# Kernel tuning notes

Hardware: AMD Instinct MI355X
Metric: run time of the kernel (lower is better)

The kernel has to match this reference:

```python
import jax, jax.numpy as jnp
import numpy as np

N = 100000   # nodes
E = 800000   # directed edges (symmetrized to 2E in forward)
D0 = 128     # input feature dim (dim0)
H = 128      # hidden = h_dim * args.d = 64 * 2
L = 4        # num_layers
G = 64       # num graphs for global_mean_pool
BN_EPS = 1e-5
LN_EPS = 1e-5


def setup_inputs() -> dict:
    key = jax.random.key(0)
    ks = jax.random.split(key, 12)
    s = 1.0 / np.sqrt(H)
    x = jax.random.normal(ks[0], (N, D0), dtype=jnp.float32)
    row = jax.random.randint(ks[1], (E,), 0, N, dtype=jnp.int32)
    off = jax.random.randint(ks[2], (E,), 1, N, dtype=jnp.int32)
    col = (row + off) % N  # guarantees row != col (no self loops)
    edge_index = jnp.stack([row, col])
    batch = jnp.sort(jax.random.randint(ks[3], (N,), 0, G, dtype=jnp.int32))
    return {
        "x": x,
        "W0": jax.random.normal(ks[4], (D0, H), dtype=jnp.float32) * s,
        "b0": jnp.zeros((H,), jnp.float32),
        "eps_l": jnp.zeros((L,), jnp.float32),        # GIN eps per layer
        "W1": jax.random.normal(ks[5], (L, H, H), dtype=jnp.float32) * s,
        "b1": jnp.zeros((L, H), jnp.float32),
        "bn_g": jnp.ones((L, H), jnp.float32),
        "bn_b": jnp.zeros((L, H), jnp.float32),
        "W2": jax.random.normal(ks[6], (L, H, H), dtype=jnp.float32) * s,
        "b2": jnp.zeros((L, H), jnp.float32),
        "ln_g": jnp.ones((L, H), jnp.float32),
        "ln_b": jnp.zeros((L, H), jnp.float32),
        "edge_index": edge_index,
        "batch": batch,
    }


def reference(x, W0, b0, eps_l, W1, b1, bn_g, bn_b, W2, b2, ln_g, ln_b, edge_index, batch):
    n = x.shape[0]
    h = x @ W0 + b0  # layer0 encode -> [N, H]
    # FNSD: symmetrize edges (cat with flip) and drop self loops
    ei = jnp.concatenate([edge_index, edge_index[::-1]], axis=1)
    row, col = ei[0], ei[1]
    w = (row != col).astype(h.dtype)  # self-loop removal as zero edge weight
    for i in range(L):
        # GINConv: scatter-add of neighbor features
        agg = jax.ops.segment_sum(w[:, None] * h[col], row, num_segments=n)
        u = (1.0 + eps_l[i]) * h + agg
        # mlp: Linear -> BatchNorm1d (training-mode batch stats) -> ReLU -> Linear
        z = u @ W1[i] + b1[i]
        m = jnp.mean(z, axis=0)
        v = jnp.var(z, axis=0)
        z = (z - m) * jax.lax.rsqrt(v + BN_EPS) * bn_g[i] + bn_b[i]
        z = jax.nn.relu(z)
        z = z @ W2[i] + b2[i]
        z = jax.nn.relu(z)          # use_activation
        h = h + z                    # use_residual
        mu = jnp.mean(h, axis=-1, keepdims=True)   # LayerNorm
        var = jnp.var(h, axis=-1, keepdims=True)
        h = (h - mu) * jax.lax.rsqrt(var + LN_EPS) * ln_g[i] + ln_b[i]
    # global_mean_pool over graph ids
    cnt = jax.ops.segment_sum(jnp.ones((n,), h.dtype), batch, num_segments=G)
    sums = jax.ops.segment_sum(h, batch, num_segments=G)
    return sums / jnp.maximum(cnt, 1.0)[:, None]
```

## Files before the change

### kernel.cpp

```cpp
#include <hip/hip_runtime.h>

#define NN 100000
#define EE 800000
#define HH 128
#define LL 4
#define GG 64
#define BN_EPS 1e-5f
#define LN_EPS 1e-5f
#define POOL_CHUNK 64
#define NBUK ((NN + 255) >> 8)
#define CAP 8192
#define BCHUNK 8192
#define UPITCH 136
#define Q8SCALE 16.0f
#define Q8INV   0.0625f

typedef __attribute__((ext_vector_type(8))) short short8;
typedef __attribute__((ext_vector_type(4))) float f32x4;

__device__ inline unsigned short bf16_rne(float f) {
    unsigned u = __float_as_uint(f);
    return (unsigned short)((u + 0x7FFF + ((u >> 16) & 1)) >> 16);
}
__device__ inline float bf16_to_f32(unsigned short h) {
    return __uint_as_float((unsigned)h << 16);
}


__global__ void setup_kernel(const float* __restrict__ W0, const float* __restrict__ W1,
                             const float* __restrict__ W2, short* __restrict__ wt_hi,
                             int* __restrict__ bcur, float* __restrict__ colsum,
                             float* __restrict__ psum, float* __restrict__ pcnt) {
    int i = blockIdx.x * 256 + threadIdx.x;
    if (i < NBUK) bcur[i] = i * CAP;
    if (i < LL * HH * 2) colsum[i] = 0.f;
    if (i < GG * HH) psum[i] = 0.f;
    if (i < GG) pcnt[i] = 0.f;
    if (i < 9 * HH * HH) {
        int mat = i >> 14, rem = i & 16383;
        int n = rem >> 7, k = rem & 127;
        const float* src = (mat == 0) ? W0 : ((mat <= 4) ? W1 + (size_t)(mat - 1) * HH * HH
                                                         : W2 + (size_t)(mat - 5) * HH * HH);
        float v = src[(size_t)k * HH + n];
        int off = (mat << 14) + (((k >> 3) * 8 + (n >> 4)) << 7) + ((n & 15) << 3) + (k & 7);
        wt_hi[off] = (short)bf16_rne(v);
    }
}


__global__ __launch_bounds__(256) void bucket_scatter(const int* __restrict__ ei, int* __restrict__ bcur,
                                                      int* __restrict__ pairs) {
    __shared__ int h[NBUK];
    __shared__ int curb[NBUK];
    int tid = threadIdx.x;
    for (int i = tid; i < NBUK; i += 256) h[i] = 0;
    __syncthreads();
    int base = blockIdx.x * BCHUNK;
#pragma unroll 4
    for (int k = 0; k < BCHUNK / 256; k++) {
        int e = base + k * 256 + tid;
        if (e < 2 * EE) {
            int r = ei[e];
            int c = (e < EE) ? ei[e + EE] : ei[e - EE];
            if (r != c) atomicAdd(&h[r >> 8], 1);
        }
    }
    __syncthreads();
    for (int i = tid; i < NBUK; i += 256) {
        int n = h[i];
        curb[i] = n ? atomicAdd(&bcur[i], n) : 0;
    }
    __syncthreads();
#pragma unroll 4
    for (int k = 0; k < BCHUNK / 256; k++) {
        int e = base + k * 256 + tid;
        if (e < 2 * EE) {
            int r = ei[e];
            int c = (e < EE) ? ei[e + EE] : ei[e - EE];
            if (r != c) {
                int p = atomicAdd(&curb[r >> 8], 1);
                pairs[p] = ((r & 255) << 17) | c;
            }
        }
    }
}

__global__ __launch_bounds__(256) void bucket_build(const int* __restrict__ pairs, const int* __restrict__ bcur,
                                                    int* __restrict__ rp, int* __restrict__ re,
                                                    int* __restrict__ colidx) {
    __shared__ int hist[256], off[256], lcol[CAP];
    int b = blockIdx.x, tid = threadIdx.x;
    int s = b * CAP;
    int size = bcur[b] - s;
    hist[tid] = 0;
    __syncthreads();
    for (int i = tid; i < size; i += 256) atomicAdd(&hist[pairs[s + i] >> 17], 1);
    __syncthreads();
    off[tid] = hist[tid];
    __syncthreads();
    for (int o = 1; o < 256; o <<= 1) {
        int x = (tid >= o) ? off[tid - o] : 0;
        __syncthreads();
        off[tid] += x;
        __syncthreads();
    }
    int excl = (tid > 0) ? off[tid - 1] : 0;
    int r = (b << 8) + tid;
    if (r < NN) { rp[r] = s + excl; re[r] = s + off[tid]; }
    hist[tid] = excl;
    __syncthreads();
    for (int i = tid; i < size; i += 256) {
        int u = pairs[s + i];
        int p = atomicAdd(&hist[u >> 17], 1);
        lcol[p] = u & 0x1FFFF;
    }
    __syncthreads();
    for (int i = tid; i < size; i += 256) colidx[s + i] = lcol[i];
}


__global__ __launch_bounds__(256, 6) void fused_g1(
    const uint2* __restrict__ hbf2,
    const unsigned int* __restrict__ h8,
    const int* __restrict__ rp, const int* __restrict__ re,
    const int* __restrict__ colidx,
    const float* __restrict__ eps_l, int layer,
    const short* __restrict__ wt,
    const float* __restrict__ bias,
    unsigned short* __restrict__ z1_out,
    float* __restrict__ colsum, float* __restrict__ colsq)
{
    __shared__ __align__(16) unsigned short uls[64 * UPITCH];
    __shared__ float stats[2 * HH];
    int tid = threadIdx.x;
    int wave = tid >> 6, lane = tid & 63;
    int half = lane >> 5, sub = lane & 31;
    int lrow = lane & 15, kgrp = lane >> 4;
    int r0 = blockIdx.x * 64;
    stats[tid] = 0.f;
    float eps1 = 1.0f + eps_l[layer];

    int hw = wave * 2 + half;
    for (int rl = 0; rl < 8; rl++) {
        int row = hw * 8 + rl;
        int r = r0 + row;
        float a0 = 0.f, a1 = 0.f, a2 = 0.f, a3 = 0.f;
        uint2 sv = make_uint2(0u, 0u);
        if (r < NN) {
            sv = hbf2[(size_t)r * 32 + sub];
            int base = rp[r];
            int n = re[r] - base;
            for (int i = 0; i < n; i += 8) {
                unsigned v[8];
                int c[8];
#pragma unroll
                for (int j = 0; j < 8; j++) c[j] = (i + j < n) ? colidx[base + i + j] : -1;
#pragma unroll
                for (int j = 0; j < 8; j++)
                    v[j] = (c[j] >= 0) ? h8[(size_t)c[j] * 32 + sub] : 0u;
#pragma unroll
                for (int j = 0; j < 8; j++) {
                    a0 += (float)((int)(v[j] << 24) >> 24);
                    a1 += (float)((int)(v[j] << 16) >> 24);
                    a2 += (float)((int)(v[j] <<  8) >> 24);
                    a3 += (float)((int)v[j] >> 24);
                }
            }
        }
        a0 = fmaf(bf16_to_f32((unsigned short)(sv.x & 0xFFFF)), eps1, a0 * Q8INV);
        a1 = fmaf(bf16_to_f32((unsigned short)(sv.x >> 16)),    eps1, a1 * Q8INV);
        a2 = fmaf(bf16_to_f32((unsigned short)(sv.y & 0xFFFF)), eps1, a2 * Q8INV);
        a3 = fmaf(bf16_to_f32((unsigned short)(sv.y >> 16)),    eps1, a3 * Q8INV);
        uint2 o;
        o.x = (unsigned)bf16_rne(a0) | ((unsigned)bf16_rne(a1) << 16);
        o.y = (unsigned)bf16_rne(a2) | ((unsigned)bf16_rne(a3) << 16);
        *(uint2*)&uls[row * UPITCH + sub * 4] = o;
    }
    __syncthreads();

    short8 az[4];
#pragma unroll
    for (int ks = 0; ks < 4; ks++)
        az[ks] = *(const short8*)&uls[(wave * 16 + lrow) * UPITCH + ks * 32 + kgrp * 8];
    __syncthreads();

    f32x4 acc[8];
#pragma unroll
    for (int c = 0; c < 8; c++) acc[c] = (f32x4){0.f, 0.f, 0.f, 0.f};
#pragma unroll
    for (int ks = 0; ks < 4; ks++) {
        int fb = (ks * 4 + kgrp) * 8;
#pragma unroll
        for (int c = 0; c < 8; c++) {
            short8 whi = *(const short8*)(wt + (size_t)((fb + c) << 7) + (lrow << 3));
            acc[c] = __builtin_amdgcn_mfma_f32_16x16x32_bf16(az[ks], whi, acc[c], 0, 0, 0);
        }
    }

    float bv[8];
#pragma unroll
    for (int c = 0; c < 8; c++) bv[c] = bias[c * 16 + lrow];
    int lrb = wave * 16 + kgrp * 4;
    float ps[8], pq[8];
#pragma unroll
    for (int c = 0; c < 8; c++) { ps[c] = 0.f; pq[c] = 0.f; }
#pragma unroll
    for (int c = 0; c < 8; c++)
#pragma unroll
        for (int reg = 0; reg < 4; reg++) {
            float z = acc[c][reg] + bv[c];
            uls[(lrb + reg) * UPITCH + c * 16 + lrow] = bf16_rne(z);
            if (r0 + lrb + reg < NN) { ps[c] += z; pq[c] += z * z; }
        }
#pragma unroll
    for (int c = 0; c < 8; c++) {
        ps[c] += __shfl_xor(ps[c], 16); pq[c] += __shfl_xor(pq[c], 16);
        ps[c] += __shfl_xor(ps[c], 32); pq[c] += __shfl_xor(pq[c], 32);
    }
    if (kgrp == 0) {
#pragma unroll
        for (int c = 0; c < 8; c++) {
            atomicAdd(&stats[c * 16 + lrow], ps[c]);
            atomicAdd(&stats[HH + c * 16 + lrow], pq[c]);
        }
    }
    __syncthreads();
#pragma unroll
    for (int i = 0; i < 4; i++) {
        int idx = tid + i * 256;
        int row = idx >> 4;
        int r = r0 + row;
        if (r < NN)
            *(uint4*)(z1_out + (size_t)r * HH + (idx & 15) * 8) =
                *(const uint4*)&uls[row * UPITCH + (idx & 15) * 8];
    }
    if (tid < HH) {
        atomicAdd(&colsum[tid], stats[tid]);
        atomicAdd(&colsq[tid], stats[HH + tid]);
    }
}


template<int MODE>
__global__ __launch_bounds__(256, 4) void gemm_v9(
    const void* __restrict__ Ain,
    const short* __restrict__ wt_hi,
    const float* __restrict__ bias,
    float* __restrict__ colsum, float* __restrict__ colsq,
    const float* __restrict__ bng, const float* __restrict__ bnb,
    const float* __restrict__ lng, const float* __restrict__ lnb,
    unsigned short* __restrict__ hbf,
    unsigned int* __restrict__ h8out)
{
    __shared__ short wh[HH * HH];
    __shared__ float stats[2 * HH];
    int tid = threadIdx.x;
    int wave = tid >> 6, lane = tid & 63;
    int lrow = lane & 15, kgrp = lane >> 4;
    int r0 = blockIdx.x * 64;
    int arow = r0 + wave * 16 + lrow;

    {
        const short8* src = (const short8*)wt_hi;
        short8* dst = (short8*)wh;
#pragma unroll
        for (int i = 0; i < 8; i++) dst[tid + i * 256] = src[tid + i * 256];
    }
    if (MODE == 2 && tid < HH) {
        float m = colsum[tid] * (1.f / NN);
        float v = colsq[tid] * (1.f / NN) - m * m;
        float a = bng[tid] * rsqrtf(v + BN_EPS);
        stats[tid] = a;
        stats[HH + tid] = bnb[tid] - m * a;
    }

    float4 a0[4], a1[4];
    short8 az[4];
    if (MODE == 2) {
        const unsigned short* Az = (const unsigned short*)Ain;
        if (arow < NN) {
#pragma unroll
            for (int ks = 0; ks < 4; ks++)
                az[ks] = *(const short8*)(Az + (size_t)arow * HH + ks * 32 + kgrp * 8);
        } else {
#pragma unroll
            for (int ks = 0; ks < 4; ks++) az[ks] = (short8){0,0,0,0,0,0,0,0};
        }
    } else {
        const float* Af = (const float*)Ain;
        if (arow < NN) {
#pragma unroll
            for (int ks = 0; ks < 4; ks++) {
                int kb = ks * 32 + kgrp * 8;
                a0[ks] = *(const float4*)(Af + (size_t)arow * HH + kb);
                a1[ks] = *(const float4*)(Af + (size_t)arow * HH + kb + 4);
            }
        } else {
#pragma unroll
            for (int ks = 0; ks < 4; ks++) {
                a0[ks] = make_float4(0.f, 0.f, 0.f, 0.f);
                a1[ks] = a0[ks];
            }
        }
    }
    __syncthreads();

    f32x4 acc[8];
#pragma unroll
    for (int c = 0; c < 8; c++) acc[c] = (f32x4){0.f, 0.f, 0.f, 0.f};

#pragma unroll
    for (int ks = 0; ks < 4; ks++) {
        int fb = (ks * 4 + kgrp) * 8;
        int kb = ks * 32 + kgrp * 8;
        float av[8];
        if (MODE == 2) {
#pragma unroll
            for (int j = 0; j < 8; j++) {
                float zb = bf16_to_f32((unsigned short)az[ks][j]);
                av[j] = fmaxf(fmaf(zb, stats[kb + j], stats[HH + kb + j]), 0.f);
            }
        } else {
            av[0] = a0[ks].x; av[1] = a0[ks].y; av[2] = a0[ks].z; av[3] = a0[ks].w;
            av[4] = a1[ks].x; av[5] = a1[ks].y; av[6] = a1[ks].z; av[7] = a1[ks].w;
        }
        short8 ahi, alo;
#pragma unroll
        for (int j = 0; j < 8; j++) {
            unsigned short hb = bf16_rne(av[j]);
            ahi[j] = (short)hb;
            alo[j] = (short)bf16_rne(av[j] - bf16_to_f32(hb));
        }
#pragma unroll
        for (int c = 0; c < 8; c++) {
            short8 whi = *(const short8*)(wh + ((fb + c) << 7) + (lrow << 3));
            acc[c] = __builtin_amdgcn_mfma_f32_16x16x32_bf16(ahi, whi, acc[c], 0, 0, 0);
            acc[c] = __builtin_amdgcn_mfma_f32_16x16x32_bf16(alo, whi, acc[c], 0, 0, 0);
        }
    }

    float bv[8];
#pragma unroll
    for (int c = 0; c < 8; c++) bv[c] = bias[c * 16 + lrow];
    int lrb = wave * 16 + kgrp * 4;
    unsigned short* hst = (unsigned short*)wh;

    if (MODE == 0) {
        __syncthreads();
#pragma unroll
        for (int c = 0; c < 8; c++)
#pragma unroll
            for (int reg = 0; reg < 4; reg++)
                hst[(lrb + reg) * HH + c * 16 + lrow] = bf16_rne(acc[c][reg] + bv[c]);
        __syncthreads();
#pragma unroll
        for (int i = 0; i < 4; i++) {
            int idx = tid + i * 256;
            int r = r0 + (idx >> 4);
            if (r < NN)
                *(uint4*)(hbf + (size_t)r * HH + (idx & 15) * 8) = ((const uint4*)wh)[idx];
        }
    } else {
        float lg[8], lb[8];
#pragma unroll
        for (int c = 0; c < 8; c++) {
            lg[c] = lng[c * 16 + lrow];
            lb[c] = lnb[c * 16 + lrow];
        }
        __syncthreads();
#pragma unroll
        for (int i = 0; i < 4; i++) {
            int idx = tid + i * 256;
            int r = r0 + (idx >> 4);
            uint4 v = make_uint4(0, 0, 0, 0);
            if (r < NN) v = *(const uint4*)(hbf + (size_t)r * HH + (idx & 15) * 8);
            ((uint4*)wh)[idx] = v;
        }
        __syncthreads();
#pragma unroll
        for (int reg = 0; reg < 4; reg++) {
            int r = r0 + lrb + reg;
            if (r < NN) {
                float tv[8];
                float s = 0.f, q = 0.f;
#pragma unroll
                for (int c = 0; c < 8; c++) {
                    float hold = bf16_to_f32(hst[(lrb + reg) * HH + c * 16 + lrow]);
                    tv[c] = hold + fmaxf(acc[c][reg] + bv[c], 0.f);
                    s += tv[c]; q += tv[c] * tv[c];
                }
#pragma unroll
                for (int m = 1; m < 16; m <<= 1) {
                    s += __shfl_xor(s, m);
                    q += __shfl_xor(q, m);
                }
                float mu = s * (1.f / 128.f);
                float var = q * (1.f / 128.f) - mu * mu;
                float rs = rsqrtf(var + LN_EPS);
#pragma unroll
                for (int c = 0; c < 8; c++)
                    hst[(lrb + reg) * HH + c * 16 + lrow] =
                        bf16_rne((tv[c] - mu) * rs * lg[c] + lb[c]);
            }
        }
        __syncthreads();
#pragma unroll
        for (int i = 0; i < 4; i++) {
            int idx = tid + i * 256;
            int r = r0 + (idx >> 4);
            if (r < NN)
                *(uint4*)(hbf + (size_t)r * HH + (idx & 15) * 8) = ((const uint4*)wh)[idx];
        }
    }

    if (h8out) {
#pragma unroll
        for (int i = 0; i < 2; i++) {
            int idx = tid + i * 256;
            int row = idx >> 3, q = idx & 7;
            int r = r0 + row;
            if (r < NN) {
                unsigned w[4];
#pragma unroll
                for (int k = 0; k < 4; k++) {
                    uint2 d = *(const uint2*)&hst[row * HH + q * 16 + k * 4];
                    float f0 = bf16_to_f32((unsigned short)(d.x & 0xFFFF));
                    float f1 = bf16_to_f32((unsigned short)(d.x >> 16));
                    float f2 = bf16_to_f32((unsigned short)(d.y & 0xFFFF));
                    float f3 = bf16_to_f32((unsigned short)(d.y >> 16));
                    int q0 = (int)rintf(fminf(fmaxf(f0 * Q8SCALE, -127.f), 127.f));
                    int q1 = (int)rintf(fminf(fmaxf(f1 * Q8SCALE, -127.f), 127.f));
                    int q2 = (int)rintf(fminf(fmaxf(f2 * Q8SCALE, -127.f), 127.f));
                    int q3 = (int)rintf(fminf(fmaxf(f3 * Q8SCALE, -127.f), 127.f));
                    w[k] = (unsigned)(q0 & 255) | ((unsigned)(q1 & 255) << 8) |
                           ((unsigned)(q2 & 255) << 16) | ((unsigned)(q3 & 255) << 24);
                }
                *(uint4*)(h8out + (size_t)r * 32 + q * 4) = make_uint4(w[0], w[1], w[2], w[3]);
            }
        }
    }
}


__global__ void pool_kernel(const unsigned short* __restrict__ h, const int* __restrict__ batch,
                            float* __restrict__ psum, float* __restrict__ pcnt)
{
    int t = threadIdx.x;
    int n0 = blockIdx.x * POOL_CHUNK;
    int n1 = n0 + POOL_CHUNK; if (n1 > NN) n1 = NN;
    if (n0 >= NN) return;
    float acc = 0.f;
    int cur = batch[n0];
    int cnt = 0;
    for (int n = n0; n < n1; n++) {
        int g = batch[n];
        if (g != cur) {
            atomicAdd(&psum[cur * HH + t], acc);
            if (t == 0) atomicAdd(&pcnt[cur], (float)cnt);
            acc = 0.f; cnt = 0; cur = g;
        }
        acc += bf16_to_f32(h[(size_t)n * HH + t]);
        cnt++;
    }
    atomicAdd(&psum[cur * HH + t], acc);
    if (t == 0) atomicAdd(&pcnt[cur], (float)cnt);
}

__global__ void pool_final(const float* __restrict__ psum, const float* __restrict__ pcnt,
                           float* __restrict__ out)
{
    int i = blockIdx.x * blockDim.x + threadIdx.x;
    if (i < GG * HH) {
        float c = pcnt[i >> 7];
        out[i] = psum[i] / fmaxf(c, 1.f);
    }
}


extern "C" void kernel_launch(void* const* d_in, const int* in_sizes, int n_in,
                              void* d_out, int out_size, void* d_ws, size_t ws_size,
                              hipStream_t stream)
{
    const float* x     = (const float*)d_in[0];
    const float* W0    = (const float*)d_in[1];
    const float* b0    = (const float*)d_in[2];
    const float* eps_l = (const float*)d_in[3];
    const float* W1    = (const float*)d_in[4];
    const float* b1    = (const float*)d_in[5];
    const float* bng   = (const float*)d_in[6];
    const float* bnb   = (const float*)d_in[7];
    const float* W2    = (const float*)d_in[8];
    const float* b2    = (const float*)d_in[9];
    const float* lng   = (const float*)d_in[10];
    const float* lnb   = (const float*)d_in[11];
    const int*   ei    = (const int*)d_in[12];
    const int*   batch = (const int*)d_in[13];
    float* out = (float*)d_out;

    char* ws = (char*)d_ws;
    size_t off = 0;
    auto alloc = [&](size_t bytes) -> void* {
        void* p = ws + off;
        off += (bytes + 255) & ~(size_t)255;
        return p;
    };
    unsigned short* hbf = (unsigned short*)alloc((size_t)NN * HH * 2);
    unsigned short* z1  = (unsigned short*)alloc((size_t)NN * HH * 2);
    unsigned int*   h8  = (unsigned int*)alloc((size_t)NN * HH);
    int*   colidx = (int*)alloc((size_t)NBUK * CAP * 4 + 1024);
    int*   pairs  = (int*)alloc((size_t)NBUK * CAP * 4);
    int*   rp     = (int*)alloc((size_t)NN * 4);
    int*   re     = (int*)alloc((size_t)NN * 4);
    int*   bcur   = (int*)alloc((NBUK + 1) * 4);
    float* colsum = (float*)alloc((size_t)LL * HH * 2 * 4);
    float* psum   = (float*)alloc((size_t)GG * HH * 4);
    float* pcnt   = (float*)alloc(GG * 4);
    short* wt_hi  = (short*)alloc((size_t)9 * HH * HH * 2);

    setup_kernel<<<(9 * HH * HH + 255) / 256, 256, 0, stream>>>(W0, W1, W2, wt_hi, bcur,
                                                                colsum, psum, pcnt);

    bucket_scatter<<<(2 * EE + BCHUNK - 1) / BCHUNK, 256, 0, stream>>>(ei, bcur, pairs);
    bucket_build<<<NBUK, 256, 0, stream>>>(pairs, bcur, rp, re, colidx);

    int gb = (NN + 63) / 64;
    gemm_v9<0><<<gb, 256, 0, stream>>>(x, wt_hi, b0,
                                       nullptr, nullptr, nullptr, nullptr, nullptr, nullptr,
                                       hbf, h8);

    for (int l = 0; l < LL; l++) {
        float* cs = colsum + (size_t)l * HH * 2;
        float* cq = cs + HH;
        fused_g1<<<gb, 256, 0, stream>>>((const uint2*)hbf, h8, rp, re, colidx, eps_l, l,
                                         wt_hi + (size_t)(1 + l) * HH * HH, b1 + l * HH, z1,
                                         cs, cq);
        gemm_v9<2><<<gb, 256, 0, stream>>>(z1, wt_hi + (size_t)(5 + l) * HH * HH,
                                           b2 + l * HH,
                                           cs, cq, bng + l * HH, bnb + l * HH,
                                           lng + l * HH, lnb + l * HH, hbf,
                                           (l < LL - 1) ? h8 : nullptr);
    }

    pool_kernel<<<(NN + POOL_CHUNK - 1) / POOL_CHUNK, 128, 0, stream>>>(hbf, batch, psum, pcnt);
    pool_final<<<(GG * HH + 255) / 256, 256, 0, stream>>>(psum, pcnt, out);
}
```

Baseline: 606.9 us.

## Pad CSR rows to multiples of eight, stage indices in LDS, use packed integer accumulation

Pads each node's neighbor list to a multiple of eight, filling the padding with a dummy node whose int8 features are zero, so the gather loop drops its per-element bounds checks and loads indices as int4 vectors. Each block first copies its contiguous slice of column indices into LDS when the slice fits, and falls back to global memory otherwise. Int8 feature sums use SWAR: a bias XOR plus two 16-bit lanes in a 32-bit add, with the bias subtracted at the end, replacing per-byte float converts. The padding adds extra gather traffic against the dummy row, and the 16-bit lane sums could overflow on very high-degree nodes.

```diff
diff --git a/kernel.cpp b/kernel.cpp
--- a/kernel.cpp
+++ b/kernel.cpp
@@ -14,6 +14,7 @@
 #define UPITCH 136
 #define Q8SCALE 16.0f
 #define Q8INV   0.0625f
+#define CIDX_CAP 2048
 
 typedef __attribute__((ext_vector_type(8))) short short8;
 typedef __attribute__((ext_vector_type(4))) float f32x4;
@@ -30,12 +31,14 @@
 __global__ void setup_kernel(const float* __restrict__ W0, const float* __restrict__ W1,
                              const float* __restrict__ W2, short* __restrict__ wt_hi,
                              int* __restrict__ bcur, float* __restrict__ colsum,
-                             float* __restrict__ psum, float* __restrict__ pcnt) {
+                             float* __restrict__ psum, float* __restrict__ pcnt,
+                             unsigned int* __restrict__ h8) {
     int i = blockIdx.x * 256 + threadIdx.x;
     if (i < NBUK) bcur[i] = i * CAP;
     if (i < LL * HH * 2) colsum[i] = 0.f;
     if (i < GG * HH) psum[i] = 0.f;
     if (i < GG) pcnt[i] = 0.f;
+    if (i < 32) h8[(size_t)NN * 32 + i] = 0u;
     if (i < 9 * HH * HH) {
         int mat = i >> 14, rem = i & 16383;
         int n = rem >> 7, k = rem & 127;
@@ -85,6 +88,7 @@
     }
 }
 
+
 __global__ __launch_bounds__(256) void bucket_build(const int* __restrict__ pairs, const int* __restrict__ bcur,
                                                     int* __restrict__ rp, int* __restrict__ re,
                                                     int* __restrict__ colidx) {
@@ -93,10 +97,12 @@
     int s = b * CAP;
     int size = bcur[b] - s;
     hist[tid] = 0;
+    for (int i = tid; i < CAP; i += 256) lcol[i] = NN;
     __syncthreads();
     for (int i = tid; i < size; i += 256) atomicAdd(&hist[pairs[s + i] >> 17], 1);
     __syncthreads();
-    off[tid] = hist[tid];
+    int p = (hist[tid] + 7) & ~7;
+    off[tid] = p;
     __syncthreads();
     for (int o = 1; o < 256; o <<= 1) {
         int x = (tid >= o) ? off[tid - o] : 0;
@@ -104,18 +110,19 @@
         off[tid] += x;
         __syncthreads();
     }
-    int excl = (tid > 0) ? off[tid - 1] : 0;
+    int pexcl = off[tid] - p;
     int r = (b << 8) + tid;
-    if (r < NN) { rp[r] = s + excl; re[r] = s + off[tid]; }
-    hist[tid] = excl;
+    if (r < NN) { rp[r] = s + pexcl; re[r] = s + pexcl + p; }
+    hist[tid] = pexcl;
     __syncthreads();
     for (int i = tid; i < size; i += 256) {
         int u = pairs[s + i];
-        int p = atomicAdd(&hist[u >> 17], 1);
-        lcol[p] = u & 0x1FFFF;
-    }
-    __syncthreads();
-    for (int i = tid; i < size; i += 256) colidx[s + i] = lcol[i];
+        int pos = atomicAdd(&hist[u >> 17], 1);
+        lcol[pos] = u & 0x1FFFF;
+    }
+    __syncthreads();
+    int ptot = off[255];
+    for (int i = tid; i < ptot; i += 256) colidx[s + i] = lcol[i];
 }
 
 
@@ -131,6 +138,7 @@
     float* __restrict__ colsum, float* __restrict__ colsq)
 {
     __shared__ __align__(16) unsigned short uls[64 * UPITCH];
+    __shared__ __align__(16) int cidx[CIDX_CAP];
     __shared__ float stats[2 * HH];
     int tid = threadIdx.x;
     int wave = tid >> 6, lane = tid & 63;
@@ -140,37 +148,79 @@
     stats[tid] = 0.f;
     float eps1 = 1.0f + eps_l[layer];
 
+    int lastr = r0 + 63; if (lastr >= NN) lastr = NN - 1;
+    int blkBase = rp[r0];
+    int blkSize = re[lastr] - blkBase;
+    bool ldsOk = (blkSize <= CIDX_CAP);
+    if (ldsOk) {
+        const int4* src = (const int4*)(colidx + blkBase);
+        for (int i = tid; i * 4 < blkSize; i += 256) ((int4*)cidx)[i] = src[i];
+    }
+    __syncthreads();
+
     int hw = wave * 2 + half;
     for (int rl = 0; rl < 8; rl++) {
         int row = hw * 8 + rl;
         int r = r0 + row;
-        float a0 = 0.f, a1 = 0.f, a2 = 0.f, a3 = 0.f;
         uint2 sv = make_uint2(0u, 0u);
+        unsigned accLo = 0u, accHi = 0u;
+        int npad = 0;
         if (r < NN) {
             sv = hbf2[(size_t)r * 32 + sub];
             int base = rp[r];
-            int n = re[r] - base;
-            for (int i = 0; i < n; i += 8) {
-                unsigned v[8];
-                int c[8];
-#pragma unroll
-                for (int j = 0; j < 8; j++) c[j] = (i + j < n) ? colidx[base + i + j] : -1;
-#pragma unroll
-                for (int j = 0; j < 8; j++)
-                    v[j] = (c[j] >= 0) ? h8[(size_t)c[j] * 32 + sub] : 0u;
-#pragma unroll
-                for (int j = 0; j < 8; j++) {
-                    a0 += (float)((int)(v[j] << 24) >> 24);
-                    a1 += (float)((int)(v[j] << 16) >> 24);
-                    a2 += (float)((int)(v[j] <<  8) >> 24);
-                    a3 += (float)((int)v[j] >> 24);
+            npad = re[r] - base;
+            if (ldsOk) {
+                int lo = base - blkBase;
+                for (int i = 0; i < npad; i += 8) {
+                    int4 i0 = *(const int4*)&cidx[lo + i];
+                    int4 i1 = *(const int4*)&cidx[lo + i + 4];
+                    unsigned v[8];
+                    v[0] = h8[(size_t)i0.x * 32 + sub];
+                    v[1] = h8[(size_t)i0.y * 32 + sub];
+                    v[2] = h8[(size_t)i0.z * 32 + sub];
+                    v[3] = h8[(size_t)i0.w * 32 + sub];
+                    v[4] = h8[(size_t)i1.x * 32 + sub];
+                    v[5] = h8[(size_t)i1.y * 32 + sub];
+                    v[6] = h8[(size_t)i1.z * 32 + sub];
+                    v[7] = h8[(size_t)i1.w * 32 + sub];
+#pragma unroll
+                    for (int j = 0; j < 8; j++) {
+                        unsigned b = v[j] ^ 0x80808080u;
+                        accLo += b & 0x00FF00FFu;
+                        accHi += (b >> 8) & 0x00FF00FFu;
+                    }
                 }
-            }
-        }
-        a0 = fmaf(bf16_to_f32((unsigned short)(sv.x & 0xFFFF)), eps1, a0 * Q8INV);
-        a1 = fmaf(bf16_to_f32((unsigned short)(sv.x >> 16)),    eps1, a1 * Q8INV);
-        a2 = fmaf(bf16_to_f32((unsigned short)(sv.y & 0xFFFF)), eps1, a2 * Q8INV);
-        a3 = fmaf(bf16_to_f32((unsigned short)(sv.y >> 16)),    eps1, a3 * Q8INV);
+            } else {
+                for (int i = 0; i < npad; i += 8) {
+                    int4 i0 = *(const int4*)&colidx[base + i];
+                    int4 i1 = *(const int4*)&colidx[base + i + 4];
+                    unsigned v[8];
+                    v[0] = h8[(size_t)i0.x * 32 + sub];
+                    v[1] = h8[(size_t)i0.y * 32 + sub];
+                    v[2] = h8[(size_t)i0.z * 32 + sub];
+                    v[3] = h8[(size_t)i0.w * 32 + sub];
+                    v[4] = h8[(size_t)i1.x * 32 + sub];
+                    v[5] = h8[(size_t)i1.y * 32 + sub];
+                    v[6] = h8[(size_t)i1.z * 32 + sub];
+                    v[7] = h8[(size_t)i1.w * 32 + sub];
+#pragma unroll
+                    for (int j = 0; j < 8; j++) {
+                        unsigned b = v[j] ^ 0x80808080u;
+                        accLo += b & 0x00FF00FFu;
+                        accHi += (b >> 8) & 0x00FF00FFu;
+                    }
+                }
+            }
+        }
+        int biasq = npad << 7;
+        float a0 = (float)((int)(accLo & 0xFFFFu) - biasq) * Q8INV;
+        float a1 = (float)((int)(accHi & 0xFFFFu) - biasq) * Q8INV;
+        float a2 = (float)((int)(accLo >> 16) - biasq) * Q8INV;
+        float a3 = (float)((int)(accHi >> 16) - biasq) * Q8INV;
+        a0 = fmaf(bf16_to_f32((unsigned short)(sv.x & 0xFFFF)), eps1, a0);
+        a1 = fmaf(bf16_to_f32((unsigned short)(sv.x >> 16)),    eps1, a1);
+        a2 = fmaf(bf16_to_f32((unsigned short)(sv.y & 0xFFFF)), eps1, a2);
+        a3 = fmaf(bf16_to_f32((unsigned short)(sv.y >> 16)),    eps1, a3);
         uint2 o;
         o.x = (unsigned)bf16_rne(a0) | ((unsigned)bf16_rne(a1) << 16);
         o.y = (unsigned)bf16_rne(a2) | ((unsigned)bf16_rne(a3) << 16);
@@ -506,7 +556,7 @@
     };
     unsigned short* hbf = (unsigned short*)alloc((size_t)NN * HH * 2);
     unsigned short* z1  = (unsigned short*)alloc((size_t)NN * HH * 2);
-    unsigned int*   h8  = (unsigned int*)alloc((size_t)NN * HH);
+    unsigned int*   h8  = (unsigned int*)alloc((size_t)(NN + 1) * HH);
     int*   colidx = (int*)alloc((size_t)NBUK * CAP * 4 + 1024);
     int*   pairs  = (int*)alloc((size_t)NBUK * CAP * 4);
     int*   rp     = (int*)alloc((size_t)NN * 4);
@@ -518,7 +568,7 @@
     short* wt_hi  = (short*)alloc((size_t)9 * HH * HH * 2);
 
     setup_kernel<<<(9 * HH * HH + 255) / 256, 256, 0, stream>>>(W0, W1, W2, wt_hi, bcur,
-                                                                colsum, psum, pcnt);
+                                                                colsum, psum, pcnt, h8);
 
     bucket_scatter<<<(2 * EE + BCHUNK - 1) / BCHUNK, 256, 0, stream>>>(ei, bcur, pairs);
     bucket_build<<<NBUK, 256, 0, stream>>>(pairs, bcur, rp, re, colidx);
```

New measurement: 617.9 us. Within noise of the previous version (+1.8%).
